# Performance work log

Measured on AMD Instinct MI355X. Metric: run time of the kernel, lower is better.

Reference implementation:

```python
import jax, jax.numpy as jnp
import numpy as np


def setup_inputs() -> dict:
    key = jax.random.key(0)
    B, C, T, F = 16, 2, 1000, 257
    k1, = jax.random.split(key, 1)
    inp = jax.random.normal(k1, (B, C, T, F, 2), dtype=jnp.float32)
    weights = jnp.ones((1, C, 1, F, 1), dtype=jnp.float32)   # init constant 1
    bias = jnp.zeros((1, C, 1, F, 1), dtype=jnp.float32)     # init constant 0
    alpha = jnp.full((1, C, F, 1), -4.0, dtype=jnp.float32)  # init constant -4
    s_1 = jnp.zeros((B, C, F, 1), dtype=jnp.float32)
    return {"input": inp, "weights": weights, "bias": bias, "alpha": alpha, "s_1": s_1}


def reference(input, weights, bias, alpha, s_1):
    # input: [B, C, T, F, 2]
    in_data2 = jnp.sum(input ** 2, axis=-1, keepdims=True)  # [B, C, T, F, 1]
    a = jax.nn.sigmoid(alpha)                               # [1, C, F, 1]

    def step(s, x):
        s = s * (1.0 - a) + x * a   # EMA over time, per (c, f)
        return s, s

    # scan over time axis -> move T to leading axis
    xs = jnp.moveaxis(in_data2, 2, 0)          # [T, B, C, F, 1]
    s_last, smooth = jax.lax.scan(step, s_1, xs)
    smooth = jnp.sqrt(jnp.moveaxis(smooth, 0, 2))  # [B, C, T, F, 1]

    res = input / (smooth + 1e-8) * weights + bias
    return res, s_last
```

## Files before the change

kernel.cpp:

```cpp
#include <hip/hip_runtime.h>

#define BB 16
#define CC 2
#define TT 1000
#define FF 257
#define NCHAIN (BB * CC * FF)
#define RES_ELEMS ((size_t)BB * CC * TT * FF * 2)

#define CPB 16
#define KCH 40
#define LCH 25

__global__ __launch_bounds__(640) void fnorm_kernel(
    const float* __restrict__ input,
    const float* __restrict__ weights,
    const float* __restrict__ bias,
    const float* __restrict__ alpha,
    const float* __restrict__ s1,
    float* __restrict__ out)
{
    const int tx = threadIdx.x;
    const int k  = threadIdx.y;
    const int chain = blockIdx.x * CPB + tx;

    const int f  = chain % FF;
    const int bc = chain / FF;
    const int c  = bc % CC;
    const int cf = c * FF + f;

    const float2* __restrict__ in2 = (const float2*)input + (size_t)bc * (TT * FF) + f;
    float2* __restrict__ out2      = (float2*)out        + (size_t)bc * (TT * FF) + f;

    const float av = 1.0f / (1.0f + __expf(-alpha[cf]));
    const float om = 1.0f - av;
    const float w  = weights[cf];
    const float bi = bias[cf];

    const int t0 = k * LCH;

    float s = 0.0f;
    float p = 1.0f;
    #pragma unroll
    for (int t = 0; t < LCH; ++t) {
        float2 v = in2[(size_t)(t0 + t) * FF];
        float d2 = fmaf(v.x, v.x, v.y * v.y);
        s = fmaf(d2, av, s * om);
        p *= om;
    }

    __shared__ float e_s[KCH][CPB];
    __shared__ float sinit_s[KCH][CPB];
    e_s[k][tx] = s;
    __syncthreads();
    if (k == 0) {
        float S = s1[chain];
        #pragma unroll
        for (int kk = 0; kk < KCH; ++kk) {
            sinit_s[kk][tx] = S;
            S = fmaf(S, p, e_s[kk][tx]);
        }
        out[RES_ELEMS + (size_t)chain] = S;
    }
    __syncthreads();

    s = sinit_s[k][tx];
    #pragma unroll
    for (int t = 0; t < LCH; ++t) {
        float2 v = in2[(size_t)(t0 + t) * FF];
        float d2 = fmaf(v.x, v.x, v.y * v.y);
        s = fmaf(d2, av, s * om);
        float inv = __frsqrt_rn(s + 1e-16f) * w;
        float2 y;
        y.x = fmaf(v.x, inv, bi);
        y.y = fmaf(v.y, inv, bi);
        out2[(size_t)(t0 + t) * FF] = y;
    }
}

extern "C" void kernel_launch(void* const* d_in, const int* in_sizes, int n_in,
                              void* d_out, int out_size, void* d_ws, size_t ws_size,
                              hipStream_t stream) {
    const float* input   = (const float*)d_in[0];
    const float* weights = (const float*)d_in[1];
    const float* bias    = (const float*)d_in[2];
    const float* alpha   = (const float*)d_in[3];
    const float* s1      = (const float*)d_in[4];
    float* out = (float*)d_out;

    dim3 block(CPB, KCH);
    dim3 grid(NCHAIN / CPB);
    hipLaunchKernelGGL(fnorm_kernel, grid, block, 0, stream,
                       input, weights, bias, alpha, s1, out);
}
```

Measured before the change: 154.3 us.

## Split EMA scan into two passes with coalesced slab staging in LDS

Replaces the single kernel, which processed 16 frequency chains per block with strided per-thread loads, with two launches. Each block stages a contiguous (time-chunk × all-frequency) slab in shared memory so global reads are fully coalesced. Pass 1 writes per-chunk partial EMA sums to workspace. Pass 2 folds the preceding chunks' partials serially to get its initial state, then normalizes and writes the output. The cost is a second full read of the input, an extra launch, and an O(k) serial combine per block.

Result: slower. 170.7 us (+10.7%).

```diff
diff --git a/kernel.cpp b/kernel.cpp
--- a/kernel.cpp
+++ b/kernel.cpp
@@ -4,76 +4,84 @@
 #define CC 2
 #define TT 1000
 #define FF 257
-#define NCHAIN (BB * CC * FF)
+#define NBC (BB * CC)
+#define LCH 25
+#define KCH 40
+#define SLAB_F2 (LCH * FF)
 #define RES_ELEMS ((size_t)BB * CC * TT * FF * 2)
+#define NTHR 320
 
-#define CPB 16
-#define KCH 40
-#define LCH 25
-
-__global__ __launch_bounds__(640) void fnorm_kernel(
+template <bool PASS2>
+__global__ __launch_bounds__(NTHR) void fnorm_pass(
     const float* __restrict__ input,
     const float* __restrict__ weights,
     const float* __restrict__ bias,
     const float* __restrict__ alpha,
     const float* __restrict__ s1,
+    float* __restrict__ e,
     float* __restrict__ out)
 {
-    const int tx = threadIdx.x;
-    const int k  = threadIdx.y;
-    const int chain = blockIdx.x * CPB + tx;
+    __shared__ float2 xs[SLAB_F2];
 
-    const int f  = chain % FF;
-    const int bc = chain / FF;
-    const int c  = bc % CC;
-    const int cf = c * FF + f;
+    const int bid = blockIdx.x;
+    const int bc  = bid / KCH;
+    const int k   = bid % KCH;
+    const int tid = threadIdx.x;
+    const int c   = bc % CC;
 
-    const float2* __restrict__ in2 = (const float2*)input + (size_t)bc * (TT * FF) + f;
-    float2* __restrict__ out2      = (float2*)out        + (size_t)bc * (TT * FF) + f;
+    const float2* __restrict__ slab =
+        (const float2*)input + ((size_t)bc * TT + (size_t)k * LCH) * FF;
+    for (int i = tid; i < SLAB_F2; i += NTHR)
+        xs[i] = slab[i];
 
-    const float av = 1.0f / (1.0f + __expf(-alpha[cf]));
-    const float om = 1.0f - av;
-    const float w  = weights[cf];
-    const float bi = bias[cf];
-
-    const int t0 = k * LCH;
-
-    float s = 0.0f;
-    float p = 1.0f;
-    #pragma unroll
-    for (int t = 0; t < LCH; ++t) {
-        float2 v = in2[(size_t)(t0 + t) * FF];
-        float d2 = fmaf(v.x, v.x, v.y * v.y);
-        s = fmaf(d2, av, s * om);
-        p *= om;
+    float av = 0.f, om = 1.f, w = 0.f, bi = 0.f, S = 0.f;
+    const int f = tid;
+    if (f < FF) {
+        const int cf = c * FF + f;
+        av = 1.0f / (1.0f + __expf(-alpha[cf]));
+        om = 1.0f - av;
+        if (PASS2) {
+            w  = weights[cf];
+            bi = bias[cf];
+            float p2 = om * om, p4 = p2 * p2, p8 = p4 * p4, p16 = p8 * p8;
+            float p = p16 * p8 * om;
+            S = s1[bc * FF + f];
+            const float* __restrict__ erow = e + (size_t)bc * KCH * FF + f;
+            for (int kk = 0; kk < k; ++kk)
+                S = fmaf(S, p, erow[(size_t)kk * FF]);
+        }
     }
 
-    __shared__ float e_s[KCH][CPB];
-    __shared__ float sinit_s[KCH][CPB];
-    e_s[k][tx] = s;
-    __syncthreads();
-    if (k == 0) {
-        float S = s1[chain];
-        #pragma unroll
-        for (int kk = 0; kk < KCH; ++kk) {
-            sinit_s[kk][tx] = S;
-            S = fmaf(S, p, e_s[kk][tx]);
-        }
-        out[RES_ELEMS + (size_t)chain] = S;
-    }
     __syncthreads();
 
-    s = sinit_s[k][tx];
-    #pragma unroll
-    for (int t = 0; t < LCH; ++t) {
-        float2 v = in2[(size_t)(t0 + t) * FF];
-        float d2 = fmaf(v.x, v.x, v.y * v.y);
-        s = fmaf(d2, av, s * om);
-        float inv = __frsqrt_rn(s + 1e-16f) * w;
-        float2 y;
-        y.x = fmaf(v.x, inv, bi);
-        y.y = fmaf(v.y, inv, bi);
-        out2[(size_t)(t0 + t) * FF] = y;
+    if (f < FF) {
+        if (PASS2) {
+            float2* __restrict__ out2 =
+                (float2*)out + ((size_t)bc * TT + (size_t)k * LCH) * FF + f;
+            float s = S;
+            #pragma unroll
+            for (int t = 0; t < LCH; ++t) {
+                float2 v = xs[t * FF + f];
+                float d2 = fmaf(v.x, v.x, v.y * v.y);
+                s = fmaf(d2, av, s * om);
+                float inv = __frsqrt_rn(s + 1e-16f) * w;
+                float2 y;
+                y.x = fmaf(v.x, inv, bi);
+                y.y = fmaf(v.y, inv, bi);
+                out2[(size_t)t * FF] = y;
+            }
+            if (k == KCH - 1)
+                out[RES_ELEMS + (size_t)bc * FF + f] = s;
+        } else {
+            float s = 0.0f;
+            #pragma unroll
+            for (int t = 0; t < LCH; ++t) {
+                float2 v = xs[t * FF + f];
+                float d2 = fmaf(v.x, v.x, v.y * v.y);
+                s = fmaf(d2, av, s * om);
+            }
+            e[((size_t)bc * KCH + k) * FF + f] = s;
+        }
     }
 }
 
@@ -86,9 +94,12 @@
     const float* alpha   = (const float*)d_in[3];
     const float* s1      = (const float*)d_in[4];
     float* out = (float*)d_out;
+    float* e   = (float*)d_ws;
 
-    dim3 block(CPB, KCH);
-    dim3 grid(NCHAIN / CPB);
-    hipLaunchKernelGGL(fnorm_kernel, grid, block, 0, stream,
-                       input, weights, bias, alpha, s1, out);
+    dim3 block(NTHR);
+    dim3 grid(NBC * KCH);
+    hipLaunchKernelGGL(fnorm_pass<false>, grid, block, 0, stream,
+                       input, weights, bias, alpha, s1, e, out);
+    hipLaunchKernelGGL(fnorm_pass<true>, grid, block, 0, stream,
+                       input, weights, bias, alpha, s1, e, out);
 }
```
